# Optimization experiments

Measured on AMD Instinct MI355X. Metric: run time of the kernel, lower is better.

## Reference

```python
import jax, jax.numpy as jnp
import numpy as np

N_HEADS = 16

def setup_inputs() -> dict:
    key = jax.random.key(0)
    ks = jax.random.split(key, 5)
    D = 1024
    B, T = 4, 1024
    scale = 1.0 / np.sqrt(D)
    x = jax.random.normal(ks[0], (B, T, D), dtype=jnp.float32)
    Wq = jax.random.normal(ks[1], (D, D), dtype=jnp.float32) * scale
    Wk = jax.random.normal(ks[2], (D, D), dtype=jnp.float32) * scale
    Wv = jax.random.normal(ks[3], (D, D), dtype=jnp.float32) * scale
    Wo = jax.random.normal(ks[4], (D, D), dtype=jnp.float32) * scale
    return {"x": x, "Wq": Wq, "Wk": Wk, "Wv": Wv, "Wo": Wo}


def reference(x, Wq, Wk, Wv, Wo):
    # FLA BasedLinearAttention (mode='chunk', normalize=True, scale=1) with
    # Taylor feature map phi(u) = [1, u/d^{1/4}, (u (x) u)/sqrt(2 d)], so
    # phi(q)·phi(k) = 1 + s + s^2/2 where s = (q·k)/sqrt(d).
    B, T, D = x.shape
    H = N_HEADS
    d = D // H  # head_dim == feature_dim
    # torch Linear: y = x @ W.T (bias=False in FLA proj layers)
    q = (x @ Wq.T).reshape(B, T, H, d).transpose(0, 2, 1, 3)  # b h t d
    k = (x @ Wk.T).reshape(B, T, H, d).transpose(0, 2, 1, 3)
    v = (x @ Wv.T).reshape(B, T, H, d).transpose(0, 2, 1, 3)
    s = jnp.einsum('bhtd,bhsd->bhts', q, k) / jnp.sqrt(jnp.float32(d))
    scores = 1.0 + s + 0.5 * s * s  # always > 0 (= ((s+1)^2+1)/2)
    causal = jnp.tril(jnp.ones((T, T), dtype=bool))
    scores = jnp.where(causal, scores, 0.0)
    num = jnp.einsum('bhts,bhsd->bhtd', scores, v)
    den = jnp.sum(scores, axis=-1, keepdims=True)
    o = num / den  # b h t d
    o = o.transpose(0, 2, 1, 3).reshape(B, T, D)  # b t (h d)
    return o @ Wo.T
```

## Files before the change

kernel.cpp:

```cpp
#include <hip/hip_runtime.h>

typedef unsigned short u16;
typedef __attribute__((ext_vector_type(8))) short bf16x8;
typedef __attribute__((ext_vector_type(8))) unsigned short u16x8;
typedef __attribute__((ext_vector_type(4))) float f32x4;

#define MFMA16(a, b, c) __builtin_amdgcn_mfma_f32_16x16x32_bf16((a), (b), (c), 0, 0, 0)

__device__ __forceinline__ void gll16(const void* g, void* l) {
    __builtin_amdgcn_global_load_lds(
        (const __attribute__((address_space(1))) unsigned int*)g,
        (__attribute__((address_space(3))) unsigned int*)l, 16, 0, 0);
}

__device__ __forceinline__ u16 f2b(float f) {
    unsigned int u = __float_as_uint(f);
    u += 0x7fffu + ((u >> 16) & 1u);
    return (u16)(u >> 16);
}

__device__ __forceinline__ unsigned int pkcvt(float a, float b) {
    unsigned int r;
    asm("v_cvt_pk_bf16_f32 %0, %1, %2" : "=v"(r) : "v"(a), "v"(b));
    return r;
}

__global__ __launch_bounds__(256) void cast_all(const float* __restrict__ x,
                                                const float* __restrict__ w0,
                                                const float* __restrict__ w1,
                                                const float* __restrict__ w2,
                                                const float* __restrict__ w3,
                                                u16* __restrict__ xb,
                                                u16* __restrict__ wb) {
    const int bid = blockIdx.x;
    const float* s; u16* d; int off;
    if (bid < 2048) { s = x; d = xb; off = bid; }
    else {
        const int wi = (bid - 2048) >> 9;
        s = (wi == 0) ? w0 : (wi == 1) ? w1 : (wi == 2) ? w2 : w3;
        d = wb + (size_t)wi * 1048576;
        off = (bid - 2048) & 511;
    }
    const int i = (off * 256 + threadIdx.x) * 8;
    float4 a = *(const float4*)(s + i);
    float4 b = *(const float4*)(s + i + 4);
    *(uint4*)(d + i) = make_uint4(pkcvt(a.x, a.y), pkcvt(a.z, a.w),
                                  pkcvt(b.x, b.y), pkcvt(b.z, b.w));
}

template <int BM, int BN, int MODE, int SLOTS>
__global__ __launch_bounds__(256) void gemm_bt(const u16* __restrict__ A,
                                               const u16* __restrict__ W,
                                               void* __restrict__ Yv,
                                               u16* __restrict__ vT,
                                               int K, int ldY) {
    constexpr int MI = BM / 32, NJ = BN / 32;
    constexpr int ACH = BM / 16;
    constexpr int NPW = (BM + BN) / 64;
    __shared__ u16 As[2][SLOTS][BM * 32];
    __shared__ u16 Bs[2][SLOTS][BN * 32];
    const int t = threadIdx.x, w = t >> 6, lane = t & 63;
    const int quad = lane >> 4, m16 = lane & 15;
    const int wr = (w >> 1) * (BM / 2), wc = (w & 1) * (BN / 2);
    const int row0 = blockIdx.x * BM, col0 = blockIdx.y * BN;
    const int srow = lane >> 2, scol = (lane & 3) * 8;

    auto stage = [&](int buf, int slot, int k0) {
#pragma unroll
        for (int cc = 0; cc < NPW; ++cc) {
            const int c = w * NPW + cc;
            if (c < ACH)
                gll16(A + (size_t)(row0 + c * 16 + srow) * K + k0 + scol,
                      &As[buf][slot][c * 512]);
            else
                gll16(W + (size_t)(col0 + (c - ACH) * 16 + srow) * K + k0 + scol,
                      &Bs[buf][slot][(c - ACH) * 512]);
        }
    };

    f32x4 acc[MI][NJ];
#pragma unroll
    for (int i = 0; i < MI; ++i)
#pragma unroll
        for (int j = 0; j < NJ; ++j) acc[i][j] = (f32x4){0.f, 0.f, 0.f, 0.f};

    auto compute_tile = [&](int buf, int slot) {
        bf16x8 af[MI], bf[NJ];
#pragma unroll
        for (int i = 0; i < MI; ++i)
            af[i] = *(const bf16x8*)&As[buf][slot][(wr + i * 16 + m16) * 32 + quad * 8];
#pragma unroll
        for (int j = 0; j < NJ; ++j)
            bf[j] = *(const bf16x8*)&Bs[buf][slot][(wc + j * 16 + m16) * 32 + quad * 8];
#pragma unroll
        for (int i = 0; i < MI; ++i)
#pragma unroll
            for (int j = 0; j < NJ; ++j) acc[i][j] = MFMA16(af[i], bf[j], acc[i][j]);
    };

#pragma unroll
    for (int s = 0; s < SLOTS; ++s) stage(0, s, s * 32);
    const int ngroups = K / (32 * SLOTS);
    for (int g = 0; g < ngroups; ++g) {
        const int buf = g & 1;
        __syncthreads();
        const int kn = (g + 1) * SLOTS * 32;
        if (kn < K) {
#pragma unroll
            for (int s = 0; s < SLOTS; ++s) stage(buf ^ 1, s, kn + s * 32);
        }
#pragma unroll
        for (int s = 0; s < SLOTS; ++s) compute_tile(buf, s);
    }
    if constexpr (MODE == 0) {
#pragma unroll
        for (int i = 0; i < MI; ++i)
#pragma unroll
            for (int j = 0; j < NJ; ++j)
#pragma unroll
                for (int r = 0; r < 4; ++r)
                    ((float*)Yv)[(size_t)(row0 + wr + i * 16 + quad * 4 + r) * ldY +
                                 col0 + wc + j * 16 + m16] = acc[i][j][r];
    } else {
        if (col0 < 2048) {
            u16* qk = (u16*)Yv;
#pragma unroll
            for (int i = 0; i < MI; ++i)
#pragma unroll
                for (int j = 0; j < NJ; ++j)
#pragma unroll
                    for (int r = 0; r < 4; ++r)
                        qk[(size_t)(row0 + wr + i * 16 + quad * 4 + r) * 2048 +
                           col0 + wc + j * 16 + m16] = f2b(acc[i][j][r]);
        } else {
#pragma unroll
            for (int i = 0; i < MI; ++i) {
                const int rbase = row0 + wr + i * 16;
                const int bb = rbase >> 10;
                const int tok0 = (rbase & 1023) + quad * 4;
#pragma unroll
                for (int j = 0; j < NJ; ++j) {
                    const int vTrow = bb * 1024 + (col0 + wc + j * 16 + m16 - 2048);
                    *(uint2*)(vT + (size_t)vTrow * 1024 + tok0) =
                        make_uint2(pkcvt(acc[i][j][0], acc[i][j][1]),
                                   pkcvt(acc[i][j][2], acc[i][j][3]));
                }
            }
        }
    }
}

__global__ __launch_bounds__(256) void based_attn(const u16* __restrict__ qkm,
                                                  const u16* __restrict__ vT,
                                                  u16* __restrict__ o) {
    __shared__ u16 ks[2][2][2][64][32];
    __shared__ u16 vs[2][2][2][64][32];
    __shared__ u16 SsA[2][64][32];
    __shared__ u16 SsB[2][64][32];

    const int t = threadIdx.x, w = t >> 6, lane = t & 63;
    const int quad = lane >> 4, m16 = lane & 15;
    const int p = blockIdx.x, h = blockIdx.y, b = blockIdx.z;
    const int tA = p, tB = 15 - p;
    const int srow = lane >> 2, s8 = (lane & 3) * 8;
    const int qrow = w * 16 + m16;

    const size_t qbase = (size_t)b * 1024 * 2048 + h * 64;
    const size_t kbase = qbase + 1024;
    const size_t vbase = ((size_t)b * 1024 + h * 64) * 1024;

    bf16x8 qfA[2], qfB[2];
#pragma unroll
    for (int kd = 0; kd < 2; ++kd) {
        qfA[kd] = *(const bf16x8*)(qkm + qbase +
                   (size_t)(tA * 64 + qrow) * 2048 + kd * 32 + quad * 8);
        qfB[kd] = *(const bf16x8*)(qkm + qbase +
                   (size_t)(tB * 64 + qrow) * 2048 + kd * 32 + quad * 8);
    }

    auto stage_tile = [&](int kt, int buf, int slot) {
#pragma unroll
        for (int cc = 0; cc < 2; ++cc) {
            const int c = w * 2 + cc;
            const int blk = c >> 2, rc = c & 3;
            gll16(qkm + kbase + (size_t)(kt * 64 + rc * 16 + srow) * 2048 + blk * 32 + s8,
                  &ks[buf][slot][blk][rc * 16][0]);
            gll16(vT + vbase + (size_t)(rc * 16 + srow) * 1024 + kt * 64 + blk * 32 + s8,
                  &vs[buf][slot][blk][rc * 16][0]);
        }
    };

    bf16x8 ones;
#pragma unroll
    for (int e = 0; e < 8; ++e) ones[e] = (short)0x3F80;

    f32x4 numA[4], numB[4], denA, denB;
    denA = denB = (f32x4){0.f, 0.f, 0.f, 0.f};
#pragma unroll
    for (int j = 0; j < 4; ++j) numA[j] = numB[j] = (f32x4){0.f, 0.f, 0.f, 0.f};

    auto compute = [&](int buf, int slot, int kt) {
        const bool doA = (kt <= tA);
        f32x4 sA[4], sB[4];
#pragma unroll
        for (int jk = 0; jk < 4; ++jk)
            sA[jk] = sB[jk] = (f32x4){0.f, 0.f, 0.f, 0.f};
        __builtin_amdgcn_s_setprio(1);
#pragma unroll
        for (int kd = 0; kd < 2; ++kd)
#pragma unroll
            for (int jk = 0; jk < 4; ++jk) {
                bf16x8 af = *(const bf16x8*)&ks[buf][slot][kd][jk * 16 + m16][quad * 8];
                sB[jk] = MFMA16(af, qfB[kd], sB[jk]);
                if (doA) sA[jk] = MFMA16(af, qfA[kd], sA[jk]);
            }
        __builtin_amdgcn_s_setprio(0);
#pragma unroll
        for (int jk = 0; jk < 4; ++jk) {
            const int kl = jk * 16 + quad * 4;
            float scB[4];
#pragma unroll
            for (int r = 0; r < 4; ++r) {
                const float u = fmaf(sB[jk][r], 0.125f, 1.0f);
                scB[r] = fmaf(u * 0.5f, u, 0.5f);
            }
            if (kt == tB) {
#pragma unroll
                for (int r = 0; r < 4; ++r)
                    if (kl + r > qrow) scB[r] = 0.f;
            }
            *(uint2*)&SsB[kl >> 5][qrow][kl & 31] =
                make_uint2(pkcvt(scB[0], scB[1]), pkcvt(scB[2], scB[3]));
            if (doA) {
                float scA[4];
#pragma unroll
                for (int r = 0; r < 4; ++r) {
                    const float u = fmaf(sA[jk][r], 0.125f, 1.0f);
                    scA[r] = fmaf(u * 0.5f, u, 0.5f);
                }
                if (kt == tA) {
#pragma unroll
                    for (int r = 0; r < 4; ++r)
                        if (kl + r > qrow) scA[r] = 0.f;
                }
                *(uint2*)&SsA[kl >> 5][qrow][kl & 31] =
                    make_uint2(pkcvt(scA[0], scA[1]), pkcvt(scA[2], scA[3]));
            }
        }
        __builtin_amdgcn_s_setprio(1);
#pragma unroll
        for (int kb = 0; kb < 2; ++kb) {
            bf16x8 vf[4];
#pragma unroll
            for (int j = 0; j < 4; ++j)
                vf[j] = *(const bf16x8*)&vs[buf][slot][kb][j * 16 + m16][quad * 8];
            bf16x8 sfB = *(const bf16x8*)&SsB[kb][qrow][quad * 8];
#pragma unroll
            for (int j = 0; j < 4; ++j) numB[j] = MFMA16(sfB, vf[j], numB[j]);
            denB = MFMA16(sfB, ones, denB);
            if (doA) {
                bf16x8 sfA = *(const bf16x8*)&SsA[kb][qrow][quad * 8];
#pragma unroll
                for (int j = 0; j < 4; ++j) numA[j] = MFMA16(sfA, vf[j], numA[j]);
                denA = MFMA16(sfA, ones, denA);
            }
        }
        __builtin_amdgcn_s_setprio(0);
    };

    stage_tile(0, 0, 0);
    stage_tile(1, 0, 1);

    const int ngroups = (tB + 2) >> 1;
    for (int g = 0; g < ngroups; ++g) {
        const int buf = g & 1;
        __syncthreads();
        const int kn = (g + 1) * 2;
        if (kn <= tB) {
            stage_tile(kn, buf ^ 1, 0);
            if (kn + 1 <= tB) stage_tile(kn + 1, buf ^ 1, 1);
        }
        const int kt0 = g * 2;
        compute(buf, 0, kt0);
        if (kt0 + 1 <= tB) compute(buf, 1, kt0 + 1);
    }

#pragma unroll
    for (int r = 0; r < 4; ++r) {
        const float invA = 1.0f / denA[r], invB = 1.0f / denB[r];
        const int rowoff = w * 16 + quad * 4 + r;
        const size_t tokA = (size_t)(b * 1024 + tA * 64 + rowoff);
        const size_t tokB = (size_t)(b * 1024 + tB * 64 + rowoff);
#pragma unroll
        for (int j = 0; j < 4; ++j) {
            o[tokA * 1024 + h * 64 + j * 16 + m16] = f2b(numA[j][r] * invA);
            o[tokB * 1024 + h * 64 + j * 16 + m16] = f2b(numB[j][r] * invB);
        }
    }
}

extern "C" void kernel_launch(void* const* d_in, const int* in_sizes, int n_in,
                              void* d_out, int out_size, void* d_ws, size_t ws_size,
                              hipStream_t stream) {
    const float* x  = (const float*)d_in[0];
    const float* Wq = (const float*)d_in[1];
    const float* Wk = (const float*)d_in[2];
    const float* Wv = (const float*)d_in[3];
    const float* Wo = (const float*)d_in[4];
    float* out = (float*)d_out;

    const size_t MEL = 4096ull * 1024ull;
    u16* xb   = (u16*)d_ws;
    u16* Wqkv = xb + MEL;
    u16* Wob  = Wqkv + 3ull * 1024 * 1024;
    u16* qk   = Wob + 1024ull * 1024;
    u16* vT   = qk + 2ull * MEL;
    u16* o    = vT + MEL;

    cast_all<<<4096, 256, 0, stream>>>(x, Wq, Wk, Wv, Wo, xb, Wqkv);

    dim3 gq(32, 24);
    gemm_bt<128, 128, 1, 1><<<gq, 256, 0, stream>>>(xb, Wqkv, qk, vT, 1024, 2048);

    dim3 ga(8, 16, 4);
    based_attn<<<ga, 256, 0, stream>>>(qk, vT, o);

    dim3 go(64, 16);
    gemm_bt<64, 64, 0, 2><<<go, 256, 0, stream>>>(o, Wob, (void*)out, nullptr, 1024, 1024);
}
```

Measured before the change: 165.0 us.

## Replace QKV projection GEMM with 256x256-tile, 512-thread triple-buffered kernel

Adds a dedicated QKV GEMM kernel that uses 256x256 output tiles, 8 waves per block and a three-stage global-to-LDS pipeline synchronised with explicit vmcnt waits and barriers. It replaces the 128x128, 256-thread generic GEMM. The aim is more operand reuse per LDS load and better overlap of loads with MFMA work. In exchange the grid drops to 192 blocks, which is fewer than the CU count, and the larger accumulator tile raises register pressure and may lower occupancy.

```diff
diff --git a/kernel.cpp b/kernel.cpp
--- a/kernel.cpp
+++ b/kernel.cpp
@@ -46,6 +46,96 @@
     float4 b = *(const float4*)(s + i + 4);
     *(uint4*)(d + i) = make_uint4(pkcvt(a.x, a.y), pkcvt(a.z, a.w),
                                   pkcvt(b.x, b.y), pkcvt(b.z, b.w));
+}
+
+__global__ __launch_bounds__(512) void gemm256_qkv(const u16* __restrict__ A,
+                                                   const u16* __restrict__ W,
+                                                   u16* __restrict__ qk,
+                                                   u16* __restrict__ vT) {
+    constexpr int K = 1024, NKT = K / 32;
+    __shared__ u16 As[3][256 * 32];
+    __shared__ u16 Bs[3][256 * 32];
+    const int t = threadIdx.x, w = t >> 6, lane = t & 63;
+    const int quad = lane >> 4, m16 = lane & 15;
+    const int wr = (w >> 2) * 128, wc = (w & 3) * 64;
+    const int row0 = blockIdx.x * 256, col0 = blockIdx.y * 256;
+    const int srow = lane >> 2, scol = (lane & 3) * 8;
+
+    auto stage = [&](int buf, int k0) {
+#pragma unroll
+        for (int c = 0; c < 2; ++c)
+            gll16(A + (size_t)(row0 + c * 128 + w * 16 + srow) * K + k0 + scol,
+                  &As[buf][(c * 128 + w * 16) * 32]);
+#pragma unroll
+        for (int c = 0; c < 2; ++c)
+            gll16(W + (size_t)(col0 + c * 128 + w * 16 + srow) * K + k0 + scol,
+                  &Bs[buf][(c * 128 + w * 16) * 32]);
+    };
+
+    f32x4 acc[8][4];
+#pragma unroll
+    for (int i = 0; i < 8; ++i)
+#pragma unroll
+        for (int j = 0; j < 4; ++j) acc[i][j] = (f32x4){0.f, 0.f, 0.f, 0.f};
+
+    auto compute = [&](int buf) {
+        bf16x8 af[8], bfr[4];
+#pragma unroll
+        for (int i = 0; i < 8; ++i)
+            af[i] = *(const bf16x8*)&As[buf][(wr + i * 16 + m16) * 32 + quad * 8];
+#pragma unroll
+        for (int j = 0; j < 4; ++j)
+            bfr[j] = *(const bf16x8*)&Bs[buf][(wc + j * 16 + m16) * 32 + quad * 8];
+#pragma unroll
+        for (int i = 0; i < 8; ++i)
+#pragma unroll
+            for (int j = 0; j < 4; ++j) acc[i][j] = MFMA16(af[i], bfr[j], acc[i][j]);
+    };
+
+    stage(0, 0); stage(1, 32); stage(2, 64);
+
+    int buf = 0;
+    for (int kt = 0; kt < NKT - 2; ++kt) {
+        asm volatile("s_waitcnt vmcnt(8)" ::: "memory");
+        __builtin_amdgcn_s_barrier();
+        compute(buf);
+        __builtin_amdgcn_s_barrier();
+        if (kt + 3 < NKT) stage(buf, (kt + 3) * 32);
+        buf = (buf == 2) ? 0 : buf + 1;
+    }
+    asm volatile("s_waitcnt vmcnt(4)" ::: "memory");
+    __builtin_amdgcn_s_barrier();
+    compute(buf);
+    __builtin_amdgcn_s_barrier();
+    buf = (buf == 2) ? 0 : buf + 1;
+    asm volatile("s_waitcnt vmcnt(0)" ::: "memory");
+    __builtin_amdgcn_s_barrier();
+    compute(buf);
+
+    if (col0 < 2048) {
+#pragma unroll
+        for (int i = 0; i < 8; ++i)
+#pragma unroll
+            for (int j = 0; j < 4; ++j)
+#pragma unroll
+                for (int r = 0; r < 4; ++r)
+                    qk[(size_t)(row0 + wr + i * 16 + quad * 4 + r) * 2048 +
+                       col0 + wc + j * 16 + m16] = f2b(acc[i][j][r]);
+    } else {
+#pragma unroll
+        for (int i = 0; i < 8; ++i) {
+            const int rbase = row0 + wr + i * 16;
+            const int bb = rbase >> 10;
+            const int tok0 = (rbase & 1023) + quad * 4;
+#pragma unroll
+            for (int j = 0; j < 4; ++j) {
+                const int vTrow = bb * 1024 + (col0 + wc + j * 16 + m16 - 2048);
+                *(uint2*)(vT + (size_t)vTrow * 1024 + tok0) =
+                    make_uint2(pkcvt(acc[i][j][0], acc[i][j][1]),
+                               pkcvt(acc[i][j][2], acc[i][j][3]));
+            }
+        }
+    }
 }
 
 template <int BM, int BN, int MODE, int SLOTS>
@@ -121,32 +211,6 @@
                 for (int r = 0; r < 4; ++r)
                     ((float*)Yv)[(size_t)(row0 + wr + i * 16 + quad * 4 + r) * ldY +
                                  col0 + wc + j * 16 + m16] = acc[i][j][r];
-    } else {
-        if (col0 < 2048) {
-            u16* qk = (u16*)Yv;
-#pragma unroll
-            for (int i = 0; i < MI; ++i)
-#pragma unroll
-                for (int j = 0; j < NJ; ++j)
-#pragma unroll
-                    for (int r = 0; r < 4; ++r)
-                        qk[(size_t)(row0 + wr + i * 16 + quad * 4 + r) * 2048 +
-                           col0 + wc + j * 16 + m16] = f2b(acc[i][j][r]);
-        } else {
-#pragma unroll
-            for (int i = 0; i < MI; ++i) {
-                const int rbase = row0 + wr + i * 16;
-                const int bb = rbase >> 10;
-                const int tok0 = (rbase & 1023) + quad * 4;
-#pragma unroll
-                for (int j = 0; j < NJ; ++j) {
-                    const int vTrow = bb * 1024 + (col0 + wc + j * 16 + m16 - 2048);
-                    *(uint2*)(vT + (size_t)vTrow * 1024 + tok0) =
-                        make_uint2(pkcvt(acc[i][j][0], acc[i][j][1]),
-                                   pkcvt(acc[i][j][2], acc[i][j][3]));
-                }
-            }
-        }
     }
 }
 
@@ -319,8 +383,8 @@
 
     cast_all<<<4096, 256, 0, stream>>>(x, Wq, Wk, Wv, Wo, xb, Wqkv);
 
-    dim3 gq(32, 24);
-    gemm_bt<128, 128, 1, 1><<<gq, 256, 0, stream>>>(xb, Wqkv, qk, vT, 1024, 2048);
+    dim3 gq(16, 12);
+    gemm256_qkv<<<gq, 512, 0, stream>>>(xb, Wqkv, qk, vT);
 
     dim3 ga(8, 16, 4);
     based_attn<<<ga, 256, 0, stream>>>(qk, vT, o);
```

Result: slower. 171.8 us (+4.2%).
